# Kernel tuning notes

Hardware: AMD Instinct MI355X
Metric: run time of the kernel (lower is better)

Reference implementation:

```python
import jax, jax.numpy as jnp
import numpy as np

# dims: O=1 templates/chains, L=384 residues, d_pair=d_bias=128, 4 heads x 32
O, L, DP, DB, H, DH = 1, 384, 128, 128, 4, 32
SCALING = 1.0 / np.sqrt(DH)


def _ln(x, g, b):
    # torch nn.LayerNorm over last dim, eps=1e-5, biased variance
    m = jnp.mean(x, axis=-1, keepdims=True)
    v = jnp.mean((x - m) ** 2, axis=-1, keepdims=True)
    return (x - m) * jax.lax.rsqrt(v + 1e-5) * g + b


def setup_inputs() -> dict:
    key = jax.random.key(0)
    ks = jax.random.split(key, 9)

    def w(k, shape, s=0.02):
        return (jax.random.normal(k, shape) * s).astype(jnp.float32)

    return {
        "pair": jax.random.normal(ks[0], (O, L, L, DP), dtype=jnp.float32),
        "bias": jax.random.normal(ks[1], (O, L, L, DB), dtype=jnp.float32),
        "ln_pair_g": jnp.ones((DP,), jnp.float32),
        "ln_pair_b": jnp.zeros((DP,), jnp.float32),
        "ln_bias_g": jnp.ones((DB,), jnp.float32),
        "ln_bias_b": jnp.zeros((DB,), jnp.float32),
        "Wq": w(ks[2], (H * DH, DP)),  # torch Linear weight layout (out, in)
        "Wk": w(ks[3], (H * DH, DP)),
        "Wv": w(ks[4], (H * DH, DP)),
        "Wb": w(ks[5], (H, DB)),
        "Wg": w(ks[6], (H * DH, DP)),
        "bg": jnp.ones((H * DH,), jnp.float32),
        "Wo": w(ks[7], (DP, H * DH)),
        "bo": w(ks[8], (DP,)),
    }


def reference(pair, bias, ln_pair_g, ln_pair_b, ln_bias_g, ln_bias_b,
              Wq, Wk, Wv, Wb, Wg, bg, Wo, bo):
    # is_row=True: swap the two L axes so attention runs along rows
    p = jnp.transpose(pair, (0, 2, 1, 3))   # [O, L, L, DP]
    bsrc = jnp.transpose(bias, (0, 2, 1, 3))  # [O, L, L, DB]

    p = _ln(p, ln_pair_g, ln_pair_b)
    bsrc = _ln(bsrc, ln_bias_g, ln_bias_b)

    q = (p @ Wq.T).reshape(O, L, L, H, DH) * SCALING
    k = (p @ Wk.T).reshape(O, L, L, H, DH) / L
    v = (p @ Wv.T).reshape(O, L, L, H, DH)
    b = bsrc @ Wb.T                         # [O, L, L, H] pairwise bias
    gate = jax.nn.sigmoid(p @ Wg.T + bg)    # [O, L, L, H*DH]

    # attention scores contracted over the non-attended axial dim n and head dim k
    attn = jnp.einsum('bnihk,bnjhk->bijh', q, k) + b
    attn = jax.nn.softmax(attn, axis=2)     # softmax over j (torch dim=-2)

    out = jnp.einsum('bijh,bnjhd->bnihd', attn, v).reshape(O, L, L, H * DH)
    out = (gate * out) @ Wo.T + bo          # [O, L, L, DP]
    return jnp.transpose(out, (0, 2, 1, 3))  # undo is_row permute
```

## Files before the change

kernel.cpp:

```cpp
#include <hip/hip_runtime.h>
#include <hip/hip_bf16.h>

#define L_DIM 384
#define DPC 128
#define NH 4
#define DHD 32
#define HD 128
#define NROWS (L_DIM*L_DIM)
#define NSPLIT 16

typedef __hip_bfloat16 bf16;
typedef __attribute__((ext_vector_type(8))) short bf8_t;
typedef __attribute__((ext_vector_type(4))) short bf4_t;
typedef __attribute__((ext_vector_type(4))) float f4_t;

__device__ __forceinline__ float bf2f(bf16 x){ return __bfloat162float(x); }
__device__ __forceinline__ bf16 f2bf(float x){ return __float2bfloat16(x); }

union bfu8 { bf8_t v; bf16 h[8]; };

__global__ __launch_bounds__(256) void k_prep(
    const float* __restrict__ Wq, const float* __restrict__ Wk, const float* __restrict__ Wv,
    const float* __restrict__ Wg, const float* __restrict__ Wo,
    bf16* __restrict__ Wqp, bf16* __restrict__ Wkp, bf16* __restrict__ Wvp,
    bf16* __restrict__ Wgp, bf16* __restrict__ Wop)
{
  const int o = blockIdx.x * 256 + threadIdx.x;
  const int j = o & 7, lane = (o >> 3) & 63, ks = (o >> 9) & 3, nt = o >> 11;
  const int src = (nt*16 + (lane & 15))*DPC + ks*32 + (lane >> 4)*8 + j;
  Wqp[o] = f2bf(Wq[src]);
  Wkp[o] = f2bf(Wk[src]);
  Wvp[o] = f2bf(Wv[src]);
  Wgp[o] = f2bf(Wg[src]);
  Wop[o] = f2bf(Wo[src]);
}

__global__ __launch_bounds__(256) void k_bias_proj(
    const float* __restrict__ bias, const float* __restrict__ lng, const float* __restrict__ lnb,
    const float* __restrict__ Wb, float* __restrict__ bscore)
{
  const int tid = threadIdx.x;
  const int wave = tid >> 6, lane = tid & 63;
  const int half = lane >> 5, l32 = lane & 31, c = l32 * 4;
  const int t = blockIdx.x * 8 + wave * 2 + half;
  const int j = t / L_DIM, i = t % L_DIM;

  const float4 g4 = *(const float4*)&lng[c];
  const float4 b4 = *(const float4*)&lnb[c];
  float4 w4[4];
  #pragma unroll
  for (int h = 0; h < 4; ++h) w4[h] = *(const float4*)&Wb[h*DPC + c];

  const float4 xv = *(const float4*)&bias[(size_t)t * DPC + c];
  float s  = xv.x + xv.y + xv.z + xv.w;
  float ss = xv.x*xv.x + xv.y*xv.y + xv.z*xv.z + xv.w*xv.w;
  #pragma unroll
  for (int off = 16; off; off >>= 1) { s += __shfl_xor(s, off, 64); ss += __shfl_xor(ss, off, 64); }
  const float mean = s * (1.f/128.f);
  const float var  = ss * (1.f/128.f) - mean*mean;
  const float rstd = rsqrtf(var + 1e-5f);
  const float y0 = (xv.x-mean)*rstd*g4.x + b4.x;
  const float y1 = (xv.y-mean)*rstd*g4.y + b4.y;
  const float y2 = (xv.z-mean)*rstd*g4.z + b4.z;
  const float y3 = (xv.w-mean)*rstd*g4.w + b4.w;

  float p[4];
  #pragma unroll
  for (int h = 0; h < 4; ++h) {
    p[h] = y0*w4[h].x + y1*w4[h].y + y2*w4[h].z + y3*w4[h].w;
    #pragma unroll
    for (int off = 16; off; off >>= 1) p[h] += __shfl_xor(p[h], off, 64);
  }
  if (l32 == 0) {
    #pragma unroll
    for (int h = 0; h < 4; ++h)
      bscore[((size_t)h*L_DIM + i)*L_DIM + j] = p[h];
  }
}

__global__ __launch_bounds__(256) void k_pair_proj(
    const float* __restrict__ pair, const float* __restrict__ lng, const float* __restrict__ lnb,
    const bf16* __restrict__ Wqp, const bf16* __restrict__ Wkp, const bf16* __restrict__ Wvp,
    const bf16* __restrict__ Wgp, const float* __restrict__ bg,
    bf16* __restrict__ qf, bf16* __restrict__ kf, bf16* __restrict__ vf, bf16* __restrict__ gatef)
{
  __shared__ __align__(16) bf16 As[64][136];
  __shared__ __align__(16) bf16 Cbuf[10240];
  #define CS(r,cc) Cbuf[(r)*136 + (cc)]
  const int tid = threadIdx.x;
  const int wave = tid >> 6, lane = tid & 63;
  const int n = blockIdx.x / 6, i0 = (blockIdx.x % 6) * 64;
  const int m = lane & 15, q4 = lane >> 4;

  {
    const int half = lane >> 5, l32 = lane & 31, c = l32 * 4;
    const float4 g4 = *(const float4*)&lng[c];
    const float4 b4 = *(const float4*)&lnb[c];
    float4 xv[8];
    #pragma unroll
    for (int rr = 0; rr < 8; ++rr) {
      int r = wave*16 + rr*2 + half;
      xv[rr] = *(const float4*)&pair[((size_t)(i0 + r)*L_DIM + n)*DPC + c];
    }
    #pragma unroll
    for (int rr = 0; rr < 8; ++rr) {
      int r = wave*16 + rr*2 + half;
      float s  = xv[rr].x + xv[rr].y + xv[rr].z + xv[rr].w;
      float ss = xv[rr].x*xv[rr].x + xv[rr].y*xv[rr].y + xv[rr].z*xv[rr].z + xv[rr].w*xv[rr].w;
      #pragma unroll
      for (int off = 16; off; off >>= 1) { s += __shfl_xor(s, off, 64); ss += __shfl_xor(ss, off, 64); }
      float mean = s * (1.f/128.f);
      float var  = ss * (1.f/128.f) - mean*mean;
      float rstd = rsqrtf(var + 1e-5f);
      union { bf16 h[4]; bf4_t v; } pk;
      pk.h[0] = f2bf((xv[rr].x-mean)*rstd*g4.x + b4.x);
      pk.h[1] = f2bf((xv[rr].y-mean)*rstd*g4.y + b4.y);
      pk.h[2] = f2bf((xv[rr].z-mean)*rstd*g4.z + b4.z);
      pk.h[3] = f2bf((xv[rr].w-mean)*rstd*g4.w + b4.w);
      *(bf4_t*)&As[r][c] = pk.v;
    }
  }
  __syncthreads();

  bf8_t afr[4];
  #pragma unroll
  for (int ks = 0; ks < 4; ++ks)
    afr[ks] = *(const bf8_t*)&As[wave*16 + m][ks*32 + q4*8];

  const bf16* Ws[4] = {Wqp, Wkp, Wvp, Wgp};
  for (int sel = 0; sel < 4; ++sel) {
    const bf16* Wp = Ws[sel];
    #pragma unroll
    for (int nt = 0; nt < 8; ++nt) {
      f4_t acc = {0.f, 0.f, 0.f, 0.f};
      #pragma unroll
      for (int ks = 0; ks < 4; ++ks) {
        bf8_t bfr = *(const bf8_t*)&Wp[(nt*4 + ks)*512 + lane*8];
        acc = __builtin_amdgcn_mfma_f32_16x16x32_bf16(afr[ks], bfr, acc, 0, 0, 0);
      }
      const int col = nt*16 + m;
      if (sel == 2) {
        #pragma unroll
        for (int reg = 0; reg < 4; ++reg)
          Cbuf[col*80 + wave*16 + q4*4 + reg] = f2bf(acc[reg]);
      } else {
        const float bgv = (sel == 3) ? bg[col] : 0.f;
        #pragma unroll
        for (int reg = 0; reg < 4; ++reg) {
          float v = acc[reg];
          if (sel == 3) v = 1.f / (1.f + __expf(-(v + bgv)));
          CS(wave*16 + q4*4 + reg, col) = f2bf(v);
        }
      }
    }
    __syncthreads();
    if (sel == 2) {
      for (int u = tid; u < 1024; u += 256) {
        int ln = u & 63, dt = (u >> 6) & 1, h = (u >> 7) & 3, Jl = u >> 9;
        bf8_t val = *(const bf8_t*)&Cbuf[(h*32 + dt*16 + (ln&15))*80 + Jl*32 + (ln>>4)*8];
        size_t dst = ((((size_t)n*NH + h)*12 + (i0>>5) + Jl)*2 + dt)*512 + (size_t)ln*8;
        *(bf8_t*)&vf[dst] = val;
      }
    } else {
      for (int u = tid; u < 1024; u += 256) {
        int Il = u >> 8, h = (u >> 6) & 3, ln = u & 63;
        bf8_t val = *(const bf8_t*)&CS(Il*16 + (ln&15), h*32 + (ln>>4)*8);
        if (sel == 3) {
          size_t dst = ((((size_t)n*24 + (i0>>4) + Il)*NH + h)*64 + ln)*8;
          *(bf8_t*)&gatef[dst] = val;
        } else {
          bf16* out = (sel == 0) ? qf : kf;
          size_t dst = ((((size_t)n*NH + h)*24 + (i0>>4) + Il)*64 + ln)*8;
          *(bf8_t*)&out[dst] = val;
        }
      }
    }
    __syncthreads();
  }
  #undef CS
}

__global__ __launch_bounds__(256) void k_qk(
    const bf16* __restrict__ qf, const bf16* __restrict__ kf, float* __restrict__ Spart)
{
  const int tid = threadIdx.x, wave = tid >> 6, lane = tid & 63;
  const int m = lane & 15, q4 = lane >> 4;
  const int b = blockIdx.x;
  const int ks = b / 36, rem = b % 36;
  const int h = rem / 9, t9 = rem % 9;
  const int i0 = (t9/3)*128, j0 = (t9%3)*128;
  const int wr = (wave >> 1)*64, wc = (wave & 1)*64;

  f4_t acc[4][4];
  #pragma unroll
  for (int a = 0; a < 4; ++a)
    #pragma unroll
    for (int c = 0; c < 4; ++c) acc[a][c] = (f4_t){0.f,0.f,0.f,0.f};

  #pragma unroll 2
  for (int kt = 0; kt < 24; ++kt) {
    const int nIdx = ks*24 + kt;
    const bf16* qb = qf + (((size_t)nIdx*NH + h)*24 + ((i0 + wr) >> 4))*512;
    const bf16* kb = kf + (((size_t)nIdx*NH + h)*24 + ((j0 + wc) >> 4))*512;
    bf8_t af[4], bfr[4];
    #pragma unroll
    for (int x = 0; x < 4; ++x) {
      af[x]  = *(const bf8_t*)&qb[x*512 + lane*8];
      bfr[x] = *(const bf8_t*)&kb[x*512 + lane*8];
    }
    #pragma unroll
    for (int mt = 0; mt < 4; ++mt)
      #pragma unroll
      for (int nt = 0; nt < 4; ++nt)
        acc[mt][nt] = __builtin_amdgcn_mfma_f32_16x16x32_bf16(af[mt], bfr[nt], acc[mt][nt], 0, 0, 0);
  }
  float* Sp = Spart + (size_t)(ks*NH + h)*L_DIM*L_DIM;
  #pragma unroll
  for (int mt = 0; mt < 4; ++mt)
    #pragma unroll
    for (int nt = 0; nt < 4; ++nt)
      #pragma unroll
      for (int reg = 0; reg < 4; ++reg) {
        int i = i0 + wr + mt*16 + q4*4 + reg;
        int j = j0 + wc + nt*16 + m;
        Sp[(size_t)i*L_DIM + j] = acc[mt][nt][reg];
      }
}

__global__ __launch_bounds__(192) void k_softmax(
    const float* __restrict__ Spart, const float* __restrict__ bscore, bf16* __restrict__ attnf)
{
  const int t = threadIdx.x, wave = t >> 6, lane = t & 63;
  const int h = blockIdx.x / L_DIM, i = blockIdx.x % L_DIM;
  const float sc = 0.17677669529663687f / 384.f;
  const size_t off = ((size_t)h*L_DIM + i)*L_DIM + t*2;

  float ax = 0.f, ay = 0.f;
  #pragma unroll
  for (int ksp = 0; ksp < NSPLIT; ++ksp) {
    float2 p = *(const float2*)&Spart[(size_t)ksp*(NH*L_DIM*L_DIM) + off];
    ax += p.x; ay += p.y;
  }
  const float2 bs = *(const float2*)&bscore[off];
  ax = ax*sc + bs.x;
  ay = ay*sc + bs.y;

  __shared__ float redm[3], reds[3];
  float mx = fmaxf(ax, ay);
  #pragma unroll
  for (int o = 32; o; o >>= 1) mx = fmaxf(mx, __shfl_xor(mx, o, 64));
  if (lane == 0) redm[wave] = mx;
  __syncthreads();
  mx = fmaxf(fmaxf(redm[0], redm[1]), redm[2]);
  float ex = __expf(ax - mx), ey = __expf(ay - mx);
  float sm = ex + ey;
  #pragma unroll
  for (int o = 32; o; o >>= 1) sm += __shfl_xor(sm, o, 64);
  if (lane == 0) reds[wave] = sm;
  __syncthreads();
  const float inv = 1.f / (reds[0] + reds[1] + reds[2]);

  const int j = t*2;
  const int I = i >> 4, mm = i & 15, J = j >> 5, q4 = (j >> 3) & 3, jj = j & 7;
  union { bf16 h2[2]; unsigned u; } pk;
  pk.h2[0] = f2bf(ex * inv);
  pk.h2[1] = f2bf(ey * inv);
  size_t a = ((((size_t)h*24 + I)*12 + J)*64 + q4*16 + mm)*8 + jj;
  *(unsigned*)&attnf[a] = pk.u;
}

__global__ __launch_bounds__(256) void k_pv(
    const bf16* __restrict__ attnf, const bf16* __restrict__ vf, const bf16* __restrict__ gatef,
    bf16* __restrict__ goutf)
{
  __shared__ __align__(16) bf16 Cs2[384*40];
  const int tid = threadIdx.x, wave = tid >> 6, lane = tid & 63;
  const int m = lane & 15, q4 = lane >> 4;
  const int n = blockIdx.x >> 2, h = blockIdx.x & 3;

  f4_t acc[6][2];
  #pragma unroll
  for (int a = 0; a < 6; ++a) { acc[a][0] = (f4_t){0,0,0,0}; acc[a][1] = (f4_t){0,0,0,0}; }

  for (int J = 0; J < 12; ++J) {
    const bf16* vb = vf + (((size_t)(n*NH + h)*12 + J)*2)*512;
    bf8_t b0 = *(const bf8_t*)&vb[lane*8];
    bf8_t b1 = *(const bf8_t*)&vb[512 + lane*8];
    #pragma unroll
    for (int mt = 0; mt < 6; ++mt) {
      const int I = wave*6 + mt;
      bf8_t af = *(const bf8_t*)&attnf[(((size_t)h*24 + I)*12 + J)*512 + (size_t)lane*8];
      acc[mt][0] = __builtin_amdgcn_mfma_f32_16x16x32_bf16(af, b0, acc[mt][0], 0, 0, 0);
      acc[mt][1] = __builtin_amdgcn_mfma_f32_16x16x32_bf16(af, b1, acc[mt][1], 0, 0, 0);
    }
  }
  #pragma unroll
  for (int mt = 0; mt < 6; ++mt)
    #pragma unroll
    for (int dt = 0; dt < 2; ++dt)
      #pragma unroll
      for (int reg = 0; reg < 4; ++reg) {
        int i_loc = 16*(wave*6 + mt) + q4*4 + reg;
        Cs2[i_loc*40 + dt*16 + m] = f2bf(acc[mt][dt][reg]);
      }
  __syncthreads();
  #pragma unroll
  for (int it = 0; it < 6; ++it) {
    int u = tid + it*256;
    int I = u >> 6, ln = u & 63;
    bfu8 uc, ug, uo;
    uc.v = *(const bf8_t*)&Cs2[(I*16 + (ln&15))*40 + (ln>>4)*8];
    size_t gidx = ((((size_t)n*24 + I)*NH + h)*64 + ln)*8;
    ug.v = *(const bf8_t*)&gatef[gidx];
    #pragma unroll
    for (int e = 0; e < 8; ++e) uo.h[e] = f2bf(bf2f(uc.h[e]) * bf2f(ug.h[e]));
    *(bf8_t*)&goutf[gidx] = uo.v;
  }
}

__global__ __launch_bounds__(256) void k_out(
    const bf16* __restrict__ goutf, const bf16* __restrict__ Wop, const float* __restrict__ bo,
    float* __restrict__ outp)
{
  __shared__ __align__(16) float Cs[64][132];
  const int tid = threadIdx.x, wave = tid >> 6, lane = tid & 63;
  const int m = lane & 15, q4 = lane >> 4;
  const int n = blockIdx.x / 6, i0 = (blockIdx.x % 6) * 64;

  bf8_t afr[4];
  #pragma unroll
  for (int ks = 0; ks < 4; ++ks)
    afr[ks] = *(const bf8_t*)&goutf[((((size_t)n*24 + (i0>>4) + wave)*NH + ks)*64 + lane)*8];

  #pragma unroll
  for (int nt = 0; nt < 8; ++nt) {
    f4_t acc = {0.f, 0.f, 0.f, 0.f};
    #pragma unroll
    for (int ks = 0; ks < 4; ++ks) {
      bf8_t bfr = *(const bf8_t*)&Wop[(nt*4 + ks)*512 + lane*8];
      acc = __builtin_amdgcn_mfma_f32_16x16x32_bf16(afr[ks], bfr, acc, 0, 0, 0);
    }
    const int col = nt*16 + m;
    const float bov = bo[col];
    #pragma unroll
    for (int reg = 0; reg < 4; ++reg)
      Cs[wave*16 + q4*4 + reg][col] = acc[reg] + bov;
  }
  __syncthreads();
  for (int u = tid; u < 2048; u += 256) {
    int r = u >> 5, c4 = (u & 31) * 4;
    size_t off = ((size_t)(i0 + r)*L_DIM + n)*DPC + c4;
    *(float4*)&outp[off] = *(const float4*)&Cs[r][c4];
  }
}

extern "C" void kernel_launch(void* const* d_in, const int* in_sizes, int n_in,
                              void* d_out, int out_size, void* d_ws, size_t ws_size,
                              hipStream_t stream)
{
  (void)in_sizes; (void)n_in; (void)out_size; (void)ws_size;
  const float* pair = (const float*)d_in[0];
  const float* bias = (const float*)d_in[1];
  const float* lnpg = (const float*)d_in[2];
  const float* lnpb = (const float*)d_in[3];
  const float* lnbg = (const float*)d_in[4];
  const float* lnbb = (const float*)d_in[5];
  const float* Wq   = (const float*)d_in[6];
  const float* Wk   = (const float*)d_in[7];
  const float* Wv   = (const float*)d_in[8];
  const float* Wb   = (const float*)d_in[9];
  const float* Wg   = (const float*)d_in[10];
  const float* bg   = (const float*)d_in[11];
  const float* Wo   = (const float*)d_in[12];
  const float* bo   = (const float*)d_in[13];
  float* outp = (float*)d_out;

  char* ws = (char*)d_ws;
  const size_t SZ = (size_t)NROWS * HD * 2;
  bf16* qfb   = (bf16*)(ws);
  bf16* kfb   = (bf16*)(ws + SZ);
  bf16* vfb   = (bf16*)(ws + 2*SZ);
  bf16* gatef = (bf16*)(ws + 3*SZ);
  float* bscore = (float*)(ws + 4*SZ);
  float* Spart  = (float*)(ws + 4*SZ + (size_t)NH*L_DIM*L_DIM*4);
  bf16*  attnf  = (bf16*)(ws + 4*SZ + (size_t)NH*L_DIM*L_DIM*4 + (size_t)NSPLIT*NH*L_DIM*L_DIM*4);
  char*  wb     = ws + 4*SZ + (size_t)NH*L_DIM*L_DIM*4 + (size_t)NSPLIT*NH*L_DIM*L_DIM*4
                     + (size_t)NH*L_DIM*L_DIM*2;
  bf16* Wqp = (bf16*)(wb);
  bf16* Wkp = (bf16*)(wb + 32768);
  bf16* Wvp = (bf16*)(wb + 65536);
  bf16* Wgp = (bf16*)(wb + 98304);
  bf16* Wop = (bf16*)(wb + 131072);
  bf16* goutf = qfb;

  hipLaunchKernelGGL(k_prep, dim3(64), dim3(256), 0, stream, Wq, Wk, Wv, Wg, Wo,
                     Wqp, Wkp, Wvp, Wgp, Wop);
  hipLaunchKernelGGL(k_bias_proj, dim3(NROWS/8), dim3(256), 0, stream, bias, lnbg, lnbb, Wb, bscore);
  hipLaunchKernelGGL(k_pair_proj, dim3(NROWS/64), dim3(256), 0, stream, pair, lnpg, lnpb,
                     Wqp, Wkp, Wvp, Wgp, bg, qfb, kfb, vfb, gatef);
  hipLaunchKernelGGL(k_qk, dim3(NSPLIT*36), dim3(256), 0, stream, qfb, kfb, Spart);
  hipLaunchKernelGGL(k_softmax, dim3(NH*L_DIM), dim3(192), 0, stream, Spart, bscore, attnf);
  hipLaunchKernelGGL(k_pv, dim3(L_DIM*NH), dim3(256), 0, stream, attnf, vfb, gatef, goutf);
  hipLaunchKernelGGL(k_out, dim3(NROWS/64), dim3(256), 0, stream, goutf, Wop, bo, outp);
}
```

Baseline: 421.7 us.

## Shrink pair-projection tiles to 32 rows and widen bias-projection rows per wave

k_pair_proj now handles 32 rows per block instead of 64. Each pair of waves shares a 16-row tile and splits the output columns between them, and a single LDS buffer is reused for the A tile and the output staging, which cuts shared memory use and doubles the grid. k_bias_proj now gives each row to 16 lanes with 8 channels per lane, so one wave covers 4 rows, the shuffle reductions are shorter and the Wb loads move inside the head loop. The intent is more occupancy and more blocks to hide the memory-bound LayerNorm loads, at the cost of an extra barrier and fewer MFMA tiles per wave.

```diff
diff --git a/kernel.cpp b/kernel.cpp
--- a/kernel.cpp
+++ b/kernel.cpp
@@ -41,37 +41,40 @@
 {
   const int tid = threadIdx.x;
   const int wave = tid >> 6, lane = tid & 63;
-  const int half = lane >> 5, l32 = lane & 31, c = l32 * 4;
-  const int t = blockIdx.x * 8 + wave * 2 + half;
+  const int sub = lane >> 4, l16 = lane & 15, c = l16 * 8;
+  const int t = blockIdx.x * 16 + wave * 4 + sub;
   const int j = t / L_DIM, i = t % L_DIM;
 
-  const float4 g4 = *(const float4*)&lng[c];
-  const float4 b4 = *(const float4*)&lnb[c];
-  float4 w4[4];
-  #pragma unroll
-  for (int h = 0; h < 4; ++h) w4[h] = *(const float4*)&Wb[h*DPC + c];
-
-  const float4 xv = *(const float4*)&bias[(size_t)t * DPC + c];
-  float s  = xv.x + xv.y + xv.z + xv.w;
-  float ss = xv.x*xv.x + xv.y*xv.y + xv.z*xv.z + xv.w*xv.w;
-  #pragma unroll
-  for (int off = 16; off; off >>= 1) { s += __shfl_xor(s, off, 64); ss += __shfl_xor(ss, off, 64); }
+  const float4 ga = *(const float4*)&lng[c], gb = *(const float4*)&lng[c+4];
+  const float4 ba = *(const float4*)&lnb[c], bb = *(const float4*)&lnb[c+4];
+  const float4 xa = *(const float4*)&bias[(size_t)t * DPC + c];
+  const float4 xb = *(const float4*)&bias[(size_t)t * DPC + c + 4];
+
+  float s  = xa.x+xa.y+xa.z+xa.w + xb.x+xb.y+xb.z+xb.w;
+  float ss = xa.x*xa.x+xa.y*xa.y+xa.z*xa.z+xa.w*xa.w
+           + xb.x*xb.x+xb.y*xb.y+xb.z*xb.z+xb.w*xb.w;
+  #pragma unroll
+  for (int off = 8; off; off >>= 1) { s += __shfl_xor(s, off, 64); ss += __shfl_xor(ss, off, 64); }
   const float mean = s * (1.f/128.f);
   const float var  = ss * (1.f/128.f) - mean*mean;
   const float rstd = rsqrtf(var + 1e-5f);
-  const float y0 = (xv.x-mean)*rstd*g4.x + b4.x;
-  const float y1 = (xv.y-mean)*rstd*g4.y + b4.y;
-  const float y2 = (xv.z-mean)*rstd*g4.z + b4.z;
-  const float y3 = (xv.w-mean)*rstd*g4.w + b4.w;
+  float y[8];
+  y[0]=(xa.x-mean)*rstd*ga.x+ba.x; y[1]=(xa.y-mean)*rstd*ga.y+ba.y;
+  y[2]=(xa.z-mean)*rstd*ga.z+ba.z; y[3]=(xa.w-mean)*rstd*ga.w+ba.w;
+  y[4]=(xb.x-mean)*rstd*gb.x+bb.x; y[5]=(xb.y-mean)*rstd*gb.y+bb.y;
+  y[6]=(xb.z-mean)*rstd*gb.z+bb.z; y[7]=(xb.w-mean)*rstd*gb.w+bb.w;
 
   float p[4];
   #pragma unroll
   for (int h = 0; h < 4; ++h) {
-    p[h] = y0*w4[h].x + y1*w4[h].y + y2*w4[h].z + y3*w4[h].w;
-    #pragma unroll
-    for (int off = 16; off; off >>= 1) p[h] += __shfl_xor(p[h], off, 64);
-  }
-  if (l32 == 0) {
+    const float4 wa = *(const float4*)&Wb[h*DPC + c];
+    const float4 wb4 = *(const float4*)&Wb[h*DPC + c + 4];
+    p[h] = y[0]*wa.x + y[1]*wa.y + y[2]*wa.z + y[3]*wa.w
+         + y[4]*wb4.x + y[5]*wb4.y + y[6]*wb4.z + y[7]*wb4.w;
+    #pragma unroll
+    for (int off = 8; off; off >>= 1) p[h] += __shfl_xor(p[h], off, 64);
+  }
+  if (l16 == 0) {
     #pragma unroll
     for (int h = 0; h < 4; ++h)
       bscore[((size_t)h*L_DIM + i)*L_DIM + j] = p[h];
@@ -84,27 +87,26 @@
     const bf16* __restrict__ Wgp, const float* __restrict__ bg,
     bf16* __restrict__ qf, bf16* __restrict__ kf, bf16* __restrict__ vf, bf16* __restrict__ gatef)
 {
-  __shared__ __align__(16) bf16 As[64][136];
-  __shared__ __align__(16) bf16 Cbuf[10240];
-  #define CS(r,cc) Cbuf[(r)*136 + (cc)]
+  __shared__ __align__(16) bf16 Sh[5120];
   const int tid = threadIdx.x;
   const int wave = tid >> 6, lane = tid & 63;
-  const int n = blockIdx.x / 6, i0 = (blockIdx.x % 6) * 64;
+  const int n = blockIdx.x / 12, i0 = (blockIdx.x % 12) * 32;
   const int m = lane & 15, q4 = lane >> 4;
+  const int rt = wave >> 1, ch = wave & 1;
 
   {
     const int half = lane >> 5, l32 = lane & 31, c = l32 * 4;
     const float4 g4 = *(const float4*)&lng[c];
     const float4 b4 = *(const float4*)&lnb[c];
-    float4 xv[8];
-    #pragma unroll
-    for (int rr = 0; rr < 8; ++rr) {
-      int r = wave*16 + rr*2 + half;
+    float4 xv[4];
+    #pragma unroll
+    for (int rr = 0; rr < 4; ++rr) {
+      int r = wave*8 + rr*2 + half;
       xv[rr] = *(const float4*)&pair[((size_t)(i0 + r)*L_DIM + n)*DPC + c];
     }
     #pragma unroll
-    for (int rr = 0; rr < 8; ++rr) {
-      int r = wave*16 + rr*2 + half;
+    for (int rr = 0; rr < 4; ++rr) {
+      int r = wave*8 + rr*2 + half;
       float s  = xv[rr].x + xv[rr].y + xv[rr].z + xv[rr].w;
       float ss = xv[rr].x*xv[rr].x + xv[rr].y*xv[rr].y + xv[rr].z*xv[rr].z + xv[rr].w*xv[rr].w;
       #pragma unroll
@@ -117,7 +119,7 @@
       pk.h[1] = f2bf((xv[rr].y-mean)*rstd*g4.y + b4.y);
       pk.h[2] = f2bf((xv[rr].z-mean)*rstd*g4.z + b4.z);
       pk.h[3] = f2bf((xv[rr].w-mean)*rstd*g4.w + b4.w);
-      *(bf4_t*)&As[r][c] = pk.v;
+      *(bf4_t*)&Sh[r*136 + c] = pk.v;
     }
   }
   __syncthreads();
@@ -125,13 +127,15 @@
   bf8_t afr[4];
   #pragma unroll
   for (int ks = 0; ks < 4; ++ks)
-    afr[ks] = *(const bf8_t*)&As[wave*16 + m][ks*32 + q4*8];
+    afr[ks] = *(const bf8_t*)&Sh[(rt*16 + m)*136 + ks*32 + q4*8];
+  __syncthreads();
 
   const bf16* Ws[4] = {Wqp, Wkp, Wvp, Wgp};
   for (int sel = 0; sel < 4; ++sel) {
     const bf16* Wp = Ws[sel];
     #pragma unroll
-    for (int nt = 0; nt < 8; ++nt) {
+    for (int ntl = 0; ntl < 4; ++ntl) {
+      const int nt = ch*4 + ntl;
       f4_t acc = {0.f, 0.f, 0.f, 0.f};
       #pragma unroll
       for (int ks = 0; ks < 4; ++ks) {
@@ -142,29 +146,29 @@
       if (sel == 2) {
         #pragma unroll
         for (int reg = 0; reg < 4; ++reg)
-          Cbuf[col*80 + wave*16 + q4*4 + reg] = f2bf(acc[reg]);
+          Sh[col*40 + rt*16 + q4*4 + reg] = f2bf(acc[reg]);
       } else {
         const float bgv = (sel == 3) ? bg[col] : 0.f;
         #pragma unroll
         for (int reg = 0; reg < 4; ++reg) {
           float v = acc[reg];
           if (sel == 3) v = 1.f / (1.f + __expf(-(v + bgv)));
-          CS(wave*16 + q4*4 + reg, col) = f2bf(v);
+          Sh[(rt*16 + q4*4 + reg)*136 + col] = f2bf(v);
         }
       }
     }
     __syncthreads();
     if (sel == 2) {
-      for (int u = tid; u < 1024; u += 256) {
-        int ln = u & 63, dt = (u >> 6) & 1, h = (u >> 7) & 3, Jl = u >> 9;
-        bf8_t val = *(const bf8_t*)&Cbuf[(h*32 + dt*16 + (ln&15))*80 + Jl*32 + (ln>>4)*8];
-        size_t dst = ((((size_t)n*NH + h)*12 + (i0>>5) + Jl)*2 + dt)*512 + (size_t)ln*8;
+      for (int u = tid; u < 512; u += 256) {
+        int ln = u & 63, dt = (u >> 6) & 1, h = u >> 7;
+        bf8_t val = *(const bf8_t*)&Sh[(h*32 + dt*16 + (ln&15))*40 + (ln>>4)*8];
+        size_t dst = ((((size_t)n*NH + h)*12 + (i0>>5))*2 + dt)*512 + (size_t)ln*8;
         *(bf8_t*)&vf[dst] = val;
       }
     } else {
-      for (int u = tid; u < 1024; u += 256) {
+      for (int u = tid; u < 512; u += 256) {
         int Il = u >> 8, h = (u >> 6) & 3, ln = u & 63;
-        bf8_t val = *(const bf8_t*)&CS(Il*16 + (ln&15), h*32 + (ln>>4)*8);
+        bf8_t val = *(const bf8_t*)&Sh[(Il*16 + (ln&15))*136 + h*32 + (ln>>4)*8];
         if (sel == 3) {
           size_t dst = ((((size_t)n*24 + (i0>>4) + Il)*NH + h)*64 + ln)*8;
           *(bf8_t*)&gatef[dst] = val;
@@ -177,7 +181,6 @@
     }
     __syncthreads();
   }
-  #undef CS
 }
 
 __global__ __launch_bounds__(256) void k_qk(
@@ -395,8 +398,8 @@
 
   hipLaunchKernelGGL(k_prep, dim3(64), dim3(256), 0, stream, Wq, Wk, Wv, Wg, Wo,
                      Wqp, Wkp, Wvp, Wgp, Wop);
-  hipLaunchKernelGGL(k_bias_proj, dim3(NROWS/8), dim3(256), 0, stream, bias, lnbg, lnbb, Wb, bscore);
-  hipLaunchKernelGGL(k_pair_proj, dim3(NROWS/64), dim3(256), 0, stream, pair, lnpg, lnpb,
+  hipLaunchKernelGGL(k_bias_proj, dim3(NROWS/16), dim3(256), 0, stream, bias, lnbg, lnbb, Wb, bscore);
+  hipLaunchKernelGGL(k_pair_proj, dim3(NROWS/32), dim3(256), 0, stream, pair, lnpg, lnpb,
                      Wqp, Wkp, Wvp, Wgp, bg, qfb, kfb, vfb, gatef);
   hipLaunchKernelGGL(k_qk, dim3(NSPLIT*36), dim3(256), 0, stream, qfb, kfb, Spart);
   hipLaunchKernelGGL(k_softmax, dim3(NH*L_DIM), dim3(192), 0, stream, Spart, bscore, attnf);
```

Measured after the change: 396.8 us. 5.9% less time.
